# Kernel tuning notes

Measured on AMD Instinct MI355X. Metric: run time of the kernel, lower is better.

## Reference

```python
import jax, jax.numpy as jnp
import numpy as np

EPS = 1e-5


def conv2d(x, w, b, groups=1):
    # x: NCHW, w: OIHW, stride 1, SAME padding (== padding=k//2 for odd k)
    y = jax.lax.conv_general_dilated(
        x, w, window_strides=(1, 1), padding='SAME',
        dimension_numbers=('NCHW', 'OIHW', 'NCHW'),
        feature_group_count=groups)
    return y + b[None, :, None, None]


def gelu(x):
    return jax.nn.gelu(x, approximate=False)  # torch default GELU is exact erf


def adaptive_feature_norm(x, gamma, beta, s1w, s1b, s2w, s2b):
    # stats_net: GAP -> 1x1 conv -> ReLU -> 1x1 conv -> chunk into (gamma_a, beta_a)
    pooled = x.mean(axis=(2, 3), keepdims=True)                 # [B,C,1,1]
    h = jax.nn.relu(conv2d(pooled, s1w, s1b))
    stats = conv2d(h, s2w, s2b)                                 # [B,2C,1,1]
    ag, ab = jnp.split(stats, 2, axis=1)
    mean = x.mean(axis=(2, 3), keepdims=True)
    n = x.shape[2] * x.shape[3]
    var = ((x - mean) ** 2).sum(axis=(2, 3), keepdims=True) / (n - 1)  # unbiased, torch.var_mean default
    x_norm = (x - mean) * jax.lax.rsqrt(var + EPS)
    return (1 + ag) * gamma * x_norm + ab * beta


def setup_inputs() -> dict:
    key = jax.random.key(0)
    ks = jax.random.split(key, 40)
    B, C, H, W = 16, 256, 96, 96
    c4 = C // 4

    def n(k, shape, s=0.02):
        return jax.random.normal(k, shape, dtype=jnp.float32) * s

    inp = dict(
        x=jax.random.normal(ks[0], (B, C, H, W), dtype=jnp.float32),
        # branch1 conv1: dim -> dim//4, 3x3
        b1_conv1_w=n(ks[1], (c4, C, 3, 3)), b1_conv1_b=jnp.zeros((c4,), jnp.float32),
        # AFN on dim//4
        afn1_gamma=jnp.ones((1, c4, 1, 1), jnp.float32), afn1_beta=jnp.zeros((1, c4, 1, 1), jnp.float32),
        afn1_s1_w=n(ks[2], (c4 // 4, c4, 1, 1)), afn1_s1_b=jnp.zeros((c4 // 4,), jnp.float32),
        afn1_s2_w=n(ks[3], (c4 * 2, c4 // 4, 1, 1)), afn1_s2_b=jnp.zeros((c4 * 2,), jnp.float32),
        # branch1 conv2: dim//4 -> dim, 3x3
        b1_conv2_w=n(ks[4], (C, c4, 3, 3)), b1_conv2_b=jnp.zeros((C,), jnp.float32),
        # AFN on dim
        afn2_gamma=jnp.ones((1, C, 1, 1), jnp.float32), afn2_beta=jnp.zeros((1, C, 1, 1), jnp.float32),
        afn2_s1_w=n(ks[5], (c4, C, 1, 1)), afn2_s1_b=jnp.zeros((c4,), jnp.float32),
        afn2_s2_w=n(ks[6], (C * 2, c4, 1, 1)), afn2_s2_b=jnp.zeros((C * 2,), jnp.float32),
        # attention qkv/proj (1x1 convs)
        qkv_w=n(ks[7], (3 * C, C, 1, 1)), qkv_b=jnp.zeros((3 * C,), jnp.float32),
        proj_w=n(ks[8], (C, C, 1, 1)), proj_b=jnp.zeros((C,), jnp.float32),
        # 3 frequency decomposition branches, stacked
        # grouped 3x3 conv: groups=C//4, in=C (4 per group), out=C//4 (1 per group) -> weight [C//4, 4, 3, 3]
        fd_dw_w=n(ks[9], (3, c4, 4, 3, 3)), fd_dw_b=jnp.zeros((3, c4), jnp.float32),
        fd_pw_w=n(ks[10], (3, C, c4, 1, 1)), fd_pw_b=jnp.zeros((3, C), jnp.float32),
        freq_weights=jnp.ones((3,), jnp.float32),
        # router: GAP -> 1x1 conv -> softmax over 2 routes
        router_w=n(ks[11], (2, C, 1, 1)), router_b=jnp.zeros((2,), jnp.float32),
    )
    return inp


def reference(x,
              b1_conv1_w, b1_conv1_b, afn1_gamma, afn1_beta, afn1_s1_w, afn1_s1_b, afn1_s2_w, afn1_s2_b,
              b1_conv2_w, b1_conv2_b, afn2_gamma, afn2_beta, afn2_s1_w, afn2_s1_b, afn2_s2_w, afn2_s2_b,
              qkv_w, qkv_b, proj_w, proj_b, fd_dw_w, fd_dw_b, fd_pw_w, fd_pw_b, freq_weights,
              router_w, router_b):
    B, C, H, W = x.shape
    num_heads = 8
    hd = C // num_heads
    scale = C ** (-0.5)

    # ---- router ----
    pooled = x.mean(axis=(2, 3), keepdims=True)
    route = jax.nn.softmax(conv2d(pooled, router_w, router_b), axis=1)  # [B,2,1,1]

    # ---- branch1: conv -> AFN -> GELU -> conv -> AFN ----
    h = conv2d(x, b1_conv1_w, b1_conv1_b)
    h = adaptive_feature_norm(h, afn1_gamma, afn1_beta, afn1_s1_w, afn1_s1_b, afn1_s2_w, afn1_s2_b)
    h = gelu(h)
    h = conv2d(h, b1_conv2_w, b1_conv2_b)
    out1 = adaptive_feature_norm(h, afn2_gamma, afn2_beta, afn2_s1_w, afn2_s1_b, afn2_s2_w, afn2_s2_b)

    # ---- branch2: multi-scale frequency attention ----
    qkv = conv2d(x, qkv_w, qkv_b).reshape(B, 3, num_heads, hd, H, W)
    q, k, v = qkv[:, 0], qkv[:, 1], qkv[:, 2]          # [B, nh, hd, H, W]
    # attn over spatial rows: q @ k^T contracts W -> [B, nh, hd, H, H]
    attn = jnp.einsum('bndhw,bndgw->bndhg', q, k) * scale
    attn = jax.nn.softmax(attn, axis=-1)
    a = jnp.einsum('bndhg,bndgw->bndhw', attn, v)       # [B, nh, hd, H, W]
    # torch: .transpose(1, 2).reshape(B, C, H, W)  (hd-major channel order)
    a = a.transpose(0, 2, 1, 3, 4).reshape(B, C, H, W)
    x_attn = conv2d(a, proj_w, proj_b)

    fw = jax.nn.softmax(freq_weights, axis=0)
    freq_out = 0.0
    for i in range(3):
        f = conv2d(x, fd_dw_w[i], fd_dw_b[i], groups=C // 4)
        f = conv2d(gelu(f), fd_pw_w[i], fd_pw_b[i])
        freq_out = freq_out + fw[i] * f
    out2 = x_attn + freq_out

    return x + route[:, 0:1, :, :] * out1 + route[:, 1:2, :, :] * out2
```

## Files before the change

### kernel.cpp

```cpp
#include <hip/hip_runtime.h>
#include <hip/hip_bf16.h>
#include <math.h>
#include <stdint.h>

#define BB 16
#define CC 256
#define C4 64
#define HH 96
#define WW 96
#define HW 9216
#define EPSF 1e-5f

using bf16x8 = __attribute__((ext_vector_type(8))) short;
using bf16x4 = __attribute__((ext_vector_type(4))) short;
using f32x4  = __attribute__((ext_vector_type(4))) float;

#define GLD16(g, l) \
    __builtin_amdgcn_global_load_lds((const __attribute__((address_space(1))) unsigned int*)(g), \
                                     (__attribute__((address_space(3))) unsigned int*)(l), 16, 0, 0)

__device__ inline float bf2f_bits(short s) {
    return __uint_as_float(((unsigned int)(unsigned short)s) << 16);
}
__device__ inline short f2bf_bits(float f) {
    unsigned int u = __float_as_uint(f);
    return (short)((u + 0x7fffu + ((u >> 16) & 1u)) >> 16);
}

__global__ void zero_n_kernel(unsigned int* __restrict__ p, int n) {
    int i = blockIdx.x * 256 + threadIdx.x;
    if (i < n) p[i] = 0u;
}

__global__ void router_kernel(const float* __restrict__ pooled, const float* __restrict__ rw,
                              const float* __restrict__ rb, const float* __restrict__ fwts,
                              float* __restrict__ route, float* __restrict__ fw) {
    int t = threadIdx.x;
    const float invhw = 1.f / (float)HW;
    if (t < BB) {
        float l0 = rb[0], l1 = rb[1];
        for (int c = 0; c < CC; ++c) {
            float p = pooled[t * CC + c] * invhw;
            l0 += p * rw[c];
            l1 += p * rw[CC + c];
        }
        float m = fmaxf(l0, l1);
        float e0 = __expf(l0 - m), e1 = __expf(l1 - m);
        float inv = 1.f / (e0 + e1);
        route[t * 2 + 0] = e0 * inv;
        route[t * 2 + 1] = e1 * inv;
    }
    if (t == BB) {
        float a = fwts[0], b = fwts[1], c = fwts[2];
        float m = fmaxf(a, fmaxf(b, c));
        float e0 = __expf(a - m), e1 = __expf(b - m), e2 = __expf(c - m);
        float inv = 1.f / (e0 + e1 + e2);
        fw[0] = e0 * inv; fw[1] = e1 * inv; fw[2] = e2 * inv;
    }
}

__global__ void pack_w3x3_kernel(const float* __restrict__ w, __hip_bfloat16* __restrict__ wt,
                                 int COUT, int CINW) {
    int idx = blockIdx.x * 256 + threadIdx.x;
    int total = COUT * 9 * CINW;
    if (idx >= total) return;
    int ci = idx % CINW; int rest = idx / CINW; int tau = rest % 9; int co = rest / 9;
    wt[idx] = __float2bfloat16(w[((size_t)co * CINW + ci) * 9 + tau]);
}

__global__ void cast_w_kernel(const float* __restrict__ w, __hip_bfloat16* __restrict__ o, int n) {
    int idx = blockIdx.x * 256 + threadIdx.x;
    if (idx < n) o[idx] = __float2bfloat16(w[idx]);
}

__global__ void cast_w448_kernel(const float* __restrict__ w, __hip_bfloat16* __restrict__ A448) {
    int idx = blockIdx.x * 256 + threadIdx.x;
    int co = idx >> 8, ci = idx & 255;
    A448[co * 448 + ci] = __float2bfloat16(w[idx]);
}

__global__ void fuse_freq_w448_kernel(const float* __restrict__ pww, const float* __restrict__ pwb,
                                      const float* __restrict__ pjb, const float* __restrict__ fw,
                                      __hip_bfloat16* __restrict__ A448, float* __restrict__ fb448) {
    int co = blockIdx.x; int t = threadIdx.x;
    int i = t >> 6, g = t & 63;
    A448[co * 448 + 256 + t] = __float2bfloat16(fw[i] * pww[((size_t)(i * 256 + co)) * 64 + g]);
    if (t == 0) fb448[co] = pjb[co] + fw[0] * pwb[co] + fw[1] * pwb[256 + co] + fw[2] * pwb[512 + co];
}

__device__ inline float to_f32(float v) { return v; }
__device__ inline float to_f32(__hip_bfloat16 v) { return __bfloat162float(v); }

template <typename TIN, int CIN, int OSTR, bool POOL>
__global__ __launch_bounds__(256) void transpose_pm_kernel(const TIN* __restrict__ x,
                                                           __hip_bfloat16* __restrict__ xt,
                                                           float* __restrict__ pooled) {
    __shared__ float s[32][33];
    __shared__ float ps[8][32];
    int p0 = blockIdx.x * 32, c0 = blockIdx.y * 32, b = blockIdx.z;
    int tx = threadIdx.x, ty = threadIdx.y;
    const TIN* xp = x + ((size_t)b * CIN + c0) * HW + p0;
#pragma unroll
    for (int i = 0; i < 4; ++i) {
        int c = ty * 4 + i;
        s[c][tx] = to_f32(xp[(size_t)c * HW + tx]);
    }
    __syncthreads();
    __hip_bfloat16* yp = xt + ((size_t)b * HW + p0) * OSTR + c0;
#pragma unroll
    for (int i = 0; i < 4; ++i) {
        int r = ty * 4 + i;
        yp[(size_t)r * OSTR + tx] = __float2bfloat16(s[tx][r]);
    }
    if (POOL) {
        float l4 = 0.f;
#pragma unroll
        for (int i = 0; i < 4; ++i) l4 += s[tx][ty * 4 + i];
        ps[ty][tx] = l4;
        __syncthreads();
        if (ty == 0) {
            float tot = 0.f;
#pragma unroll
            for (int k = 0; k < 8; ++k) tot += ps[k][tx];
            atomicAdd(&pooled[b * CIN + c0 + tx], tot);
        }
    }
}

template <int BM, int BN, int TSH, int KC, int CDIM, int EPI, int CO_TOT, bool STATS>
__global__ __launch_bounds__(256) void mfma_gemm_kernel(const short* __restrict__ A,
                                                        const short* __restrict__ Bx,
                                                        const short* __restrict__ zp,
                                                        const float* __restrict__ bias,
                                                        const float* __restrict__ route,
                                                        void* __restrict__ Y,
                                                        float* __restrict__ ssum,
                                                        float* __restrict__ sssq,
                                                        int bin0, int bout0) {
    constexpr int WM = BM / 2, WN = BN / 2;
    constexpr int FM = WM / 16, FN = WN / 16;
    constexpr int KB = KC / 32;
    constexpr int NA = BM / 16;
    constexpr int NB = BN / 16;
    __shared__ __align__(16) short As[BM * 32];
    __shared__ __align__(16) short Bs[BN * 32];
    int tid = threadIdx.x;
    int wid = tid >> 6, lane = tid & 63;
    int wy = wid >> 1, wx = wid & 1;
    int lane16 = lane & 15, quad = lane >> 4;
    int lrow = lane >> 2, lchk = lane & 3;
    int co0 = blockIdx.x * BM;
    int n0 = blockIdx.y * BN;
    int bin = blockIdx.z + bin0;
    int bout = blockIdx.z + bout0;

    f32x4 acc[FM][FN];
#pragma unroll
    for (int i = 0; i < FM; ++i)
#pragma unroll
        for (int j = 0; j < FN; ++j) acc[i][j] = (f32x4){0.f, 0.f, 0.f, 0.f};

    const short* Bbase = Bx + (size_t)bin * HW * CDIM;

    for (int tau = 0; tau < TSH; ++tau) {
        int dh = tau / 3, dw = tau % 3;
        int off = (TSH > 1) ? (dh - 1) * 96 + (dw - 1) : 0;
        for (int kb = 0; kb < KB; ++kb) {
            int kc0 = kb * 32;
#pragma unroll
            for (int t = 0; t < NA / 4; ++t) {
                int inst = wid * (NA / 4) + t;
                int row = inst * 16 + lrow;
                const short* g = A + (size_t)(co0 + row) * (TSH * KC) + tau * KC + kc0 + lchk * 8;
                GLD16(g, &As[inst * 512]);
            }
#pragma unroll
            for (int t = 0; t < NB / 4; ++t) {
                int inst = wid * (NB / 4) + t;
                int row = inst * 16 + lrow;
                int n = n0 + row;
                const short* g;
                if (TSH > 1) {
                    int h = n / 96, w = n - h * 96;
                    int hh = h + dh - 1, ww2 = w + dw - 1;
                    bool valid = ((unsigned)hh < 96u) && ((unsigned)ww2 < 96u);
                    g = valid ? (Bbase + (size_t)(n + off) * CDIM + kc0 + lchk * 8) : zp;
                } else {
                    g = Bbase + (size_t)n * CDIM + kc0 + lchk * 8;
                }
                GLD16(g, &Bs[inst * 512]);
            }
            __syncthreads();
            bf16x8 af[FM], bfr[FN];
#pragma unroll
            for (int i = 0; i < FM; ++i)
                af[i] = *(const bf16x8*)&As[(wy * WM + i * 16 + lane16) * 32 + quad * 8];
#pragma unroll
            for (int j = 0; j < FN; ++j)
                bfr[j] = *(const bf16x8*)&Bs[(wx * WN + j * 16 + lane16) * 32 + quad * 8];
#pragma unroll
            for (int i = 0; i < FM; ++i)
#pragma unroll
                for (int j = 0; j < FN; ++j)
                    acc[i][j] = __builtin_amdgcn_mfma_f32_16x16x32_bf16(af[i], bfr[j], acc[i][j], 0, 0, 0);
            __syncthreads();
        }
    }
    float scale = 1.f;
    if (EPI == 2) scale = route[bin * 2 + 1];
    float sl[FM][4], ql[FM][4];
    if (STATS) {
#pragma unroll
        for (int i = 0; i < FM; ++i)
#pragma unroll
            for (int r = 0; r < 4; ++r) { sl[i][r] = 0.f; ql[i][r] = 0.f; }
    }
#pragma unroll
    for (int i = 0; i < FM; ++i) {
        int co_l = co0 + wy * WM + i * 16 + quad * 4;
#pragma unroll
        for (int j = 0; j < FN; ++j) {
            int pix = n0 + wx * WN + j * 16 + lane16;
#pragma unroll
            for (int r = 0; r < 4; ++r) {
                int co = co_l + r;
                float v = acc[i][j][r] + bias[co];
                size_t idx = ((size_t)(bout * CO_TOT + co)) * HW + pix;
                if (EPI == 0) ((float*)Y)[idx] = v;
                else if (EPI == 1) ((__hip_bfloat16*)Y)[idx] = __float2bfloat16(v);
                else ((float*)Y)[idx] += scale * v;
                if (STATS) { sl[i][r] += v; ql[i][r] += v * v; }
            }
        }
    }
    if (STATS) {
#pragma unroll
        for (int i = 0; i < FM; ++i) {
            int co_l = co0 + wy * WM + i * 16 + quad * 4;
#pragma unroll
            for (int r = 0; r < 4; ++r) {
                float s = sl[i][r], q = ql[i][r];
                s += __shfl_xor(s, 1); q += __shfl_xor(q, 1);
                s += __shfl_xor(s, 2); q += __shfl_xor(q, 2);
                s += __shfl_xor(s, 4); q += __shfl_xor(q, 4);
                s += __shfl_xor(s, 8); q += __shfl_xor(q, 8);
                if (lane16 == 0) {
                    int bc = bout * CO_TOT + co_l + r;
                    atomicAdd(&ssum[bc], s);
                    atomicAdd(&sssq[bc], q);
                }
            }
        }
    }
}

__global__ void afn_finalize_kernel(const float* __restrict__ s, const float* __restrict__ q,
                                    float* __restrict__ mean, float* __restrict__ istd, int n) {
    int i = blockIdx.x * 256 + threadIdx.x;
    if (i >= n) return;
    float m = s[i] / (float)HW;
    float var = (q[i] - s[i] * m) / (float)(HW - 1);
    mean[i] = m;
    istd[i] = rsqrtf(var + EPSF);
}

template <int CH, int HID>
__global__ void afn_mlp_kernel(const float* __restrict__ mean,
                               const float* __restrict__ s1w, const float* __restrict__ s1b,
                               const float* __restrict__ s2w, const float* __restrict__ s2b,
                               float* __restrict__ ag, float* __restrict__ ab) {
    int b = blockIdx.x;
    __shared__ float hbuf[HID];
    int t = threadIdx.x;
    if (t < HID) {
        float s = s1b[t];
        for (int c = 0; c < CH; ++c) s += mean[b * CH + c] * s1w[t * CH + c];
        hbuf[t] = fmaxf(s, 0.f);
    }
    __syncthreads();
    if (t < 2 * CH) {
        float s = s2b[t];
#pragma unroll
        for (int k = 0; k < HID; ++k) s += hbuf[k] * s2w[t * HID + k];
        if (t < CH) ag[b * CH + t] = s;
        else        ab[b * CH + (t - CH)] = s;
    }
}

template <int CH, bool GELU>
__global__ void afn_apply_kernel(float* __restrict__ hbuf_g, const float* __restrict__ mean,
                                 const float* __restrict__ istd, const float* __restrict__ ag,
                                 const float* __restrict__ ab, const float* __restrict__ gamma,
                                 const float* __restrict__ beta) {
    int p = blockIdx.x * 256 + threadIdx.x;
    int c = blockIdx.y, b = blockIdx.z;
    int bc = b * CH + c;
    float scale = (1.f + ag[bc]) * gamma[c] * istd[bc];
    float shift = ab[bc] * beta[c];
    float m = mean[bc];
    float* ptr = hbuf_g + (size_t)bc * HW + p;
    float v = (*ptr - m) * scale + shift;
    if (GELU) v = 0.5f * v * (1.f + erff(v * 0.70710678118654752f));
    *ptr = v;
}

__global__ __launch_bounds__(256) void afn_combine_kernel(const float* __restrict__ x,
                                                          const float* __restrict__ h2,
                                                          const float* __restrict__ mean,
                                                          const float* __restrict__ istd,
                                                          const float* __restrict__ ag,
                                                          const float* __restrict__ ab,
                                                          const float* __restrict__ gamma,
                                                          const float* __restrict__ beta,
                                                          const float* __restrict__ route,
                                                          float* __restrict__ out) {
    int p4 = blockIdx.x * 256 + threadIdx.x;
    int c = blockIdx.y, b = blockIdx.z;
    int bc = b * CC + c;
    float scale = (1.f + ag[bc]) * gamma[c] * istd[bc];
    float shift = ab[bc] * beta[c];
    float m = mean[bc];
    float r0 = route[b * 2];
    size_t base = (size_t)bc * (HW / 4) + p4;
    const f32x4 xv = ((const f32x4*)x)[base];
    const f32x4 hv = ((const f32x4*)h2)[base];
    f32x4 o;
#pragma unroll
    for (int e = 0; e < 4; ++e) o[e] = xv[e] + r0 * ((hv[e] - m) * scale + shift);
    ((f32x4*)out)[base] = o;
}

__global__ __launch_bounds__(256) void vtrans_kernel(const __hip_bfloat16* __restrict__ qkv,
                                                     __hip_bfloat16* __restrict__ vt) {
    __shared__ __hip_bfloat16 s[32][34];
    int th = blockIdx.x / 3, tw = blockIdx.x % 3;
    int c = blockIdx.y, b = blockIdx.z;
    int tx = threadIdx.x, ty = threadIdx.y;
    const __hip_bfloat16* ip = qkv + ((size_t)b * 768 + 512 + c) * HW + (size_t)(th * 32) * 96 + tw * 32;
#pragma unroll
    for (int i = 0; i < 4; ++i) s[ty * 4 + i][tx] = ip[(size_t)(ty * 4 + i) * 96 + tx];
    __syncthreads();
    __hip_bfloat16* op = vt + ((size_t)b * 256 + c) * HW + (size_t)(tw * 32) * 96 + th * 32;
#pragma unroll
    for (int i = 0; i < 4; ++i) op[(size_t)(ty * 4 + i) * 96 + tx] = s[tx][ty * 4 + i];
}

__global__ __launch_bounds__(256) void attn_mfma_kernel(const __hip_bfloat16* __restrict__ qkv,
                                                        const __hip_bfloat16* __restrict__ vt,
                                                        __hip_bfloat16* __restrict__ a, int bout0) {
    int d = blockIdx.x, n = blockIdx.y, b = blockIdx.z;
    __shared__ __align__(16) __hip_bfloat16 Ps[96 * 104];
    int t = threadIdx.x;
    int lane = t & 63, wid = t >> 6;
    int wy = wid >> 1, wx = wid & 1;
    int lane16 = lane & 15, quad = lane >> 4;

    const __hip_bfloat16* qp = qkv + ((size_t)b * 768 + n * 32 + d) * HW;
    const __hip_bfloat16* kp = qp + (size_t)256 * HW;
    const __hip_bfloat16* vp = vt + ((size_t)b * 256 + n * 32 + d) * HW;

    f32x4 acc[3][3];
#pragma unroll
    for (int i = 0; i < 3; ++i)
#pragma unroll
        for (int j = 0; j < 3; ++j) acc[i][j] = (f32x4){0.f, 0.f, 0.f, 0.f};

#pragma unroll
    for (int kb = 0; kb < 3; ++kb) {
        int kc = kb * 32 + quad * 8;
        bf16x8 af[3], bfr[3];
#pragma unroll
        for (int i = 0; i < 3; ++i)
            af[i] = *(const bf16x8*)(qp + (size_t)(wy * 48 + i * 16 + lane16) * 96 + kc);
#pragma unroll
        for (int j = 0; j < 3; ++j)
            bfr[j] = *(const bf16x8*)(kp + (size_t)(wx * 48 + j * 16 + lane16) * 96 + kc);
#pragma unroll
        for (int i = 0; i < 3; ++i)
#pragma unroll
            for (int j = 0; j < 3; ++j)
                acc[i][j] = __builtin_amdgcn_mfma_f32_16x16x32_bf16(af[i], bfr[j], acc[i][j], 0, 0, 0);
    }

    const float scale = 0.0625f;
#pragma unroll
    for (int i = 0; i < 3; ++i) {
        int rbase = wy * 48 + i * 16 + quad * 4;
#pragma unroll
        for (int j = 0; j < 3; ++j) {
            int col = wx * 48 + j * 16 + lane16;
#pragma unroll
            for (int r = 0; r < 4; ++r)
                Ps[(rbase + r) * 104 + col] = __float2bfloat16(acc[i][j][r] * scale);
        }
    }
    __syncthreads();

    if (t < 192) {
        int row = t >> 1, hh = t & 1;
        const bf16x4* pr4 = (const bf16x4*)&Ps[row * 104 + hh * 48];
        float vb[48];
        float m = -1e30f;
#pragma unroll
        for (int j4 = 0; j4 < 12; ++j4) {
            bf16x4 u = pr4[j4];
#pragma unroll
            for (int e = 0; e < 4; ++e) {
                float f = bf2f_bits(u[e]);
                vb[j4 * 4 + e] = f;
                m = fmaxf(m, f);
            }
        }
        m = fmaxf(m, __shfl_xor(m, 1));
        float ssum = 0.f;
#pragma unroll
        for (int j2 = 0; j2 < 48; ++j2) { vb[j2] = __expf(vb[j2] - m); ssum += vb[j2]; }
        ssum += __shfl_xor(ssum, 1);
        float inv = 1.f / ssum;
        bf16x4* pw4 = (bf16x4*)&Ps[row * 104 + hh * 48];
#pragma unroll
        for (int j4 = 0; j4 < 12; ++j4) {
            bf16x4 o;
#pragma unroll
            for (int e = 0; e < 4; ++e) o[e] = f2bf_bits(vb[j4 * 4 + e] * inv);
            pw4[j4] = o;
        }
    }
    __syncthreads();

#pragma unroll
    for (int i = 0; i < 3; ++i)
#pragma unroll
        for (int j = 0; j < 3; ++j) acc[i][j] = (f32x4){0.f, 0.f, 0.f, 0.f};

#pragma unroll
    for (int kb = 0; kb < 3; ++kb) {
        int kc = kb * 32 + quad * 8;
        bf16x8 af[3], bfr[3];
#pragma unroll
        for (int i = 0; i < 3; ++i)
            af[i] = *(const bf16x8*)&Ps[(wy * 48 + i * 16 + lane16) * 104 + kc];
#pragma unroll
        for (int j = 0; j < 3; ++j)
            bfr[j] = *(const bf16x8*)(vp + (size_t)(wx * 48 + j * 16 + lane16) * 96 + kc);
#pragma unroll
        for (int i = 0; i < 3; ++i)
#pragma unroll
            for (int j = 0; j < 3; ++j)
                acc[i][j] = __builtin_amdgcn_mfma_f32_16x16x32_bf16(af[i], bfr[j], acc[i][j], 0, 0, 0);
    }

    __hip_bfloat16* ap = a + ((size_t)(bout0 + b) * CC + (d * 8 + n)) * HW;
#pragma unroll
    for (int i = 0; i < 3; ++i) {
        int rbase = wy * 48 + i * 16 + quad * 4;
#pragma unroll
        for (int j = 0; j < 3; ++j) {
            int col = wx * 48 + j * 16 + lane16;
#pragma unroll
            for (int r = 0; r < 4; ++r)
                ap[(size_t)(rbase + r) * 96 + col] = __float2bfloat16(acc[i][j][r]);
        }
    }
}

__global__ __launch_bounds__(256) void freq3_kernel(const float* __restrict__ x,
                                                    const float* __restrict__ dww,
                                                    const float* __restrict__ dwb,
                                                    __hip_bfloat16* __restrict__ f) {
    int p = blockIdx.x * 256 + threadIdx.x;
    int g = blockIdx.y;
    int b = blockIdx.z;
    int h = p / WW, w = p % WW;
    float a0 = dwb[g], a1 = dwb[64 + g], a2 = dwb[128 + g];
    const float* w0 = dww + g * 36;
    const float* w1 = dww + (64 + g) * 36;
    const float* w2 = dww + (128 + g) * 36;
#pragma unroll
    for (int q = 0; q < 4; ++q) {
        const float* xc = x + ((size_t)b * CC + 4 * g + q) * HW;
#pragma unroll
        for (int dh = 0; dh < 3; ++dh) {
            int hh = h + dh - 1;
            bool hv = (hh >= 0) && (hh < HH);
#pragma unroll
            for (int dw = 0; dw < 3; ++dw) {
                int ww2 = w + dw - 1;
                bool v = hv && (ww2 >= 0) && (ww2 < WW);
                float xv = v ? xc[hh * WW + ww2] : 0.f;
                int wi = q * 9 + dh * 3 + dw;
                a0 += xv * w0[wi];
                a1 += xv * w1[wi];
                a2 += xv * w2[wi];
            }
        }
    }
    a0 = 0.5f * a0 * (1.f + erff(a0 * 0.70710678118654752f));
    a1 = 0.5f * a1 * (1.f + erff(a1 * 0.70710678118654752f));
    a2 = 0.5f * a2 * (1.f + erff(a2 * 0.70710678118654752f));
    size_t base = ((size_t)b * 192 + g) * HW + p;
    f[base] = __float2bfloat16(a0);
    f[base + (size_t)64 * HW] = __float2bfloat16(a1);
    f[base + (size_t)128 * HW] = __float2bfloat16(a2);
}

extern "C" void kernel_launch(void* const* d_in, const int* in_sizes, int n_in,
                              void* d_out, int out_size, void* d_ws, size_t ws_size,
                              hipStream_t stream) {
    const float* x    = (const float*)d_in[0];
    const float* c1w  = (const float*)d_in[1];
    const float* c1b  = (const float*)d_in[2];
    const float* g1   = (const float*)d_in[3];
    const float* be1  = (const float*)d_in[4];
    const float* s1w1 = (const float*)d_in[5];
    const float* s1b1 = (const float*)d_in[6];
    const float* s2w1 = (const float*)d_in[7];
    const float* s2b1 = (const float*)d_in[8];
    const float* c2w  = (const float*)d_in[9];
    const float* c2b  = (const float*)d_in[10];
    const float* g2   = (const float*)d_in[11];
    const float* be2  = (const float*)d_in[12];
    const float* s1w2 = (const float*)d_in[13];
    const float* s1b2 = (const float*)d_in[14];
    const float* s2w2 = (const float*)d_in[15];
    const float* s2b2 = (const float*)d_in[16];
    const float* qkvw = (const float*)d_in[17];
    const float* qkvb = (const float*)d_in[18];
    const float* pjw  = (const float*)d_in[19];
    const float* pjb  = (const float*)d_in[20];
    const float* dww  = (const float*)d_in[21];
    const float* dwb  = (const float*)d_in[22];
    const float* pww  = (const float*)d_in[23];
    const float* pwb  = (const float*)d_in[24];
    const float* fwts = (const float*)d_in[25];
    const float* rw   = (const float*)d_in[26];
    const float* rb   = (const float*)d_in[27];
    float* out = (float*)d_out;
    (void)ws_size;

    char* ws = (char*)d_ws;
    float* h2 = (float*)ws;
    __hip_bfloat16* qkvs = (__hip_bfloat16*)ws;
    __hip_bfloat16* fall = (__hip_bfloat16*)ws;
    __hip_bfloat16* ftA = (__hip_bfloat16*)(ws + 56623104ULL);
    __hip_bfloat16* vt = (__hip_bfloat16*)(ws + 113246208ULL);
    float* h1 = (float*)(ws + 150994944ULL);
    __hip_bfloat16* h1t = (__hip_bfloat16*)(ws + 188743680ULL);
    __hip_bfloat16* xt = (__hip_bfloat16*)(ws + 207618048ULL);
    __hip_bfloat16* at = xt;
    const size_t TB = 283115520ULL;
    short* zp = (short*)(ws + TB);
    float* zf = (float*)(ws + TB + 256);
    float* ssum1  = zf;
    float* sssq1  = zf + 1024;
    float* ssum2  = zf + 2048;
    float* sssq2  = zf + 6144;
    float* pooled = zf + 10240;
    float* route  = zf + 14336;
    float* fw     = zf + 14368;
    float* mean1  = zf + 14372;
    float* istd1  = zf + 15396;
    float* ag1    = zf + 16420;
    float* ab1    = zf + 17444;
    float* mean2  = zf + 18468;
    float* istd2  = zf + 22564;
    float* ag2    = zf + 26660;
    float* ab2    = zf + 30756;
    float* fb448  = zf + 34852;
    char* wbase = (char*)(zf + 35108);
    __hip_bfloat16* wt1  = (__hip_bfloat16*)wbase;
    __hip_bfloat16* wt2  = (__hip_bfloat16*)(wbase + 294912);
    __hip_bfloat16* qw16 = (__hip_bfloat16*)(wbase + 589824);
    __hip_bfloat16* A448 = (__hip_bfloat16*)(wbase + 983040);

    zero_n_kernel<<<57, 256, 0, stream>>>((unsigned int*)zp, 14400);

    transpose_pm_kernel<float, 256, 256, true>
        <<<dim3(288, 8, 16), dim3(32, 8), 0, stream>>>(x, xt, pooled);
    router_kernel<<<1, 64, 0, stream>>>(pooled, rw, rb, fwts, route, fw);

    pack_w3x3_kernel<<<576, 256, 0, stream>>>(c1w, wt1, 64, 256);
    pack_w3x3_kernel<<<576, 256, 0, stream>>>(c2w, wt2, 256, 64);
    cast_w_kernel<<<768, 256, 0, stream>>>(qkvw, qw16, 768 * 256);
    cast_w448_kernel<<<256, 256, 0, stream>>>(pjw, A448);
    fuse_freq_w448_kernel<<<256, 192, 0, stream>>>(pww, pwb, pjb, fw, A448, fb448);

    mfma_gemm_kernel<64, 128, 9, 256, 256, 0, 64, true>
        <<<dim3(1, 72, 16), 256, 0, stream>>>((const short*)wt1, (const short*)xt, zp, c1b,
                                              nullptr, h1, ssum1, sssq1, 0, 0);
    afn_finalize_kernel<<<4, 256, 0, stream>>>(ssum1, sssq1, mean1, istd1, BB * C4);
    afn_mlp_kernel<64, 16><<<dim3(BB), 128, 0, stream>>>(mean1, s1w1, s1b1, s2w1, s2b1, ag1, ab1);
    afn_apply_kernel<64, true><<<dim3(36, 64, 16), 256, 0, stream>>>(h1, mean1, istd1, ag1, ab1, g1, be1);
    transpose_pm_kernel<float, 64, 64, false>
        <<<dim3(288, 2, 16), dim3(32, 8), 0, stream>>>(h1, h1t, nullptr);
    mfma_gemm_kernel<128, 128, 9, 64, 64, 0, 256, true>
        <<<dim3(2, 72, 16), 256, 0, stream>>>((const short*)wt2, (const short*)h1t, zp, c2b,
                                              nullptr, h2, ssum2, sssq2, 0, 0);
    afn_finalize_kernel<<<16, 256, 0, stream>>>(ssum2, sssq2, mean2, istd2, BB * CC);
    afn_mlp_kernel<256, 64><<<dim3(BB), 512, 0, stream>>>(mean2, s1w2, s1b2, s2w2, s2b2, ag2, ab2);
    afn_combine_kernel<<<dim3(9, 256, 16), 256, 0, stream>>>(x, h2, mean2, istd2, ag2, ab2,
                                                             g2, be2, route, out);

    for (int half = 0; half < 2; ++half) {
        mfma_gemm_kernel<128, 128, 1, 256, 256, 1, 768, false>
            <<<dim3(6, 72, 8), 256, 0, stream>>>((const short*)qw16, (const short*)xt, zp, qkvb,
                                                 nullptr, qkvs, nullptr, nullptr, half * 8, 0);
        vtrans_kernel<<<dim3(9, 256, 8), dim3(32, 8), 0, stream>>>(qkvs, vt);
        attn_mfma_kernel<<<dim3(32, 8, 8), 256, 0, stream>>>(qkvs, vt, at, half * 8);
    }

    freq3_kernel<<<dim3(36, 64, 16), 256, 0, stream>>>(x, dww, dwb, fall);

    transpose_pm_kernel<__hip_bfloat16, 256, 448, false>
        <<<dim3(288, 8, 16), dim3(32, 8), 0, stream>>>(at, ftA, nullptr);
    transpose_pm_kernel<__hip_bfloat16, 192, 448, false>
        <<<dim3(288, 6, 16), dim3(32, 8), 0, stream>>>(fall, ftA + 256, nullptr);

    mfma_gemm_kernel<128, 128, 1, 448, 448, 2, 256, false>
        <<<dim3(2, 72, 16), 256, 0, stream>>>((const short*)A448, (const short*)ftA, zp, fb448,
                                              route, out, nullptr, nullptr, 0, 0);
}
```

Before: 1.224 ms.

## Double-buffer GEMM LDS with swizzle and fuse AFN+GELU into transpose

The MFMA GEMM main loop now double-buffers LDS tiles and processes 64-wide K steps. The next stage's global-to-LDS loads are issued while the current stage computes, which halves the number of barriers. A XOR swizzle on the 16-byte chunk index is applied to both the LDS writes and reads to reduce bank conflicts. Separately, the standalone AFN-apply+GELU pass over h1 is folded into the transpose kernel, removing one full read/write of the 64-channel activation. In exchange, LDS use quadruples, which may lower occupancy, and all K dimensions must be multiples of 64.

```diff
diff --git a/kernel.cpp b/kernel.cpp
--- a/kernel.cpp
+++ b/kernel.cpp
@@ -91,10 +91,16 @@
 __device__ inline float to_f32(float v) { return v; }
 __device__ inline float to_f32(__hip_bfloat16 v) { return __bfloat162float(v); }
 
-template <typename TIN, int CIN, int OSTR, bool POOL>
+template <typename TIN, int CIN, int OSTR, bool POOL, bool AFN, bool GELU>
 __global__ __launch_bounds__(256) void transpose_pm_kernel(const TIN* __restrict__ x,
                                                            __hip_bfloat16* __restrict__ xt,
-                                                           float* __restrict__ pooled) {
+                                                           float* __restrict__ pooled,
+                                                           const float* __restrict__ mean,
+                                                           const float* __restrict__ istd,
+                                                           const float* __restrict__ ag,
+                                                           const float* __restrict__ ab,
+                                                           const float* __restrict__ gamma,
+                                                           const float* __restrict__ beta) {
     __shared__ float s[32][33];
     __shared__ float ps[8][32];
     int p0 = blockIdx.x * 32, c0 = blockIdx.y * 32, b = blockIdx.z;
@@ -103,7 +109,15 @@
 #pragma unroll
     for (int i = 0; i < 4; ++i) {
         int c = ty * 4 + i;
-        s[c][tx] = to_f32(xp[(size_t)c * HW + tx]);
+        float v = to_f32(xp[(size_t)c * HW + tx]);
+        if (AFN) {
+            int bc = b * CIN + c0 + c;
+            float sc = (1.f + ag[bc]) * gamma[c0 + c] * istd[bc];
+            float sh = ab[bc] * beta[c0 + c];
+            v = (v - mean[bc]) * sc + sh;
+            if (GELU) v = 0.5f * v * (1.f + erff(v * 0.70710678118654752f));
+        }
+        s[c][tx] = v;
     }
     __syncthreads();
     __hip_bfloat16* yp = xt + ((size_t)b * HW + p0) * OSTR + c0;
@@ -139,16 +153,18 @@
                                                         int bin0, int bout0) {
     constexpr int WM = BM / 2, WN = BN / 2;
     constexpr int FM = WM / 16, FN = WN / 16;
-    constexpr int KB = KC / 32;
+    constexpr int KBT = KC / 64;
+    constexpr int NS = TSH * KBT;
     constexpr int NA = BM / 16;
     constexpr int NB = BN / 16;
-    __shared__ __align__(16) short As[BM * 32];
-    __shared__ __align__(16) short Bs[BN * 32];
+    __shared__ __align__(16) short As[2][2][BM * 32];
+    __shared__ __align__(16) short Bs[2][2][BN * 32];
     int tid = threadIdx.x;
     int wid = tid >> 6, lane = tid & 63;
     int wy = wid >> 1, wx = wid & 1;
     int lane16 = lane & 15, quad = lane >> 4;
     int lrow = lane >> 2, lchk = lane & 3;
+    int swz = (lrow >> 1) & 3;
     int co0 = blockIdx.x * BM;
     int n0 = blockIdx.y * BN;
     int bin = blockIdx.z + bin0;
@@ -162,17 +178,21 @@
 
     const short* Bbase = Bx + (size_t)bin * HW * CDIM;
 
-    for (int tau = 0; tau < TSH; ++tau) {
+    auto stage = [&](int s, int d) {
+        int tau = (TSH > 1) ? (s / KBT) : 0;
+        int kb  = s - tau * KBT;
+        int kc0 = kb * 64;
         int dh = tau / 3, dw = tau % 3;
-        int off = (TSH > 1) ? (dh - 1) * 96 + (dw - 1) : 0;
-        for (int kb = 0; kb < KB; ++kb) {
-            int kc0 = kb * 32;
+        int off = (dh - 1) * 96 + (dw - 1);
+        int ksw = kc0 + (lchk ^ swz) * 8;
+#pragma unroll
+        for (int kk = 0; kk < 2; ++kk) {
 #pragma unroll
             for (int t = 0; t < NA / 4; ++t) {
                 int inst = wid * (NA / 4) + t;
                 int row = inst * 16 + lrow;
-                const short* g = A + (size_t)(co0 + row) * (TSH * KC) + tau * KC + kc0 + lchk * 8;
-                GLD16(g, &As[inst * 512]);
+                const short* g = A + (size_t)(co0 + row) * (TSH * KC) + tau * KC + ksw + kk * 32;
+                GLD16(g, &As[d][kk][inst * 512]);
             }
 #pragma unroll
             for (int t = 0; t < NB / 4; ++t) {
@@ -184,28 +204,44 @@
                     int h = n / 96, w = n - h * 96;
                     int hh = h + dh - 1, ww2 = w + dw - 1;
                     bool valid = ((unsigned)hh < 96u) && ((unsigned)ww2 < 96u);
-                    g = valid ? (Bbase + (size_t)(n + off) * CDIM + kc0 + lchk * 8) : zp;
+                    g = valid ? (Bbase + (size_t)(n + off) * CDIM + ksw + kk * 32) : zp;
                 } else {
-                    g = Bbase + (size_t)n * CDIM + kc0 + lchk * 8;
+                    g = Bbase + (size_t)n * CDIM + ksw + kk * 32;
                 }
-                GLD16(g, &Bs[inst * 512]);
-            }
-            __syncthreads();
+                GLD16(g, &Bs[d][kk][inst * 512]);
+            }
+        }
+    };
+
+    stage(0, 0);
+    __syncthreads();
+    for (int s = 0; s < NS; ++s) {
+        int cur = s & 1;
+        if (s + 1 < NS) stage(s + 1, cur ^ 1);
+#pragma unroll
+        for (int kk = 0; kk < 2; ++kk) {
             bf16x8 af[FM], bfr[FN];
 #pragma unroll
-            for (int i = 0; i < FM; ++i)
-                af[i] = *(const bf16x8*)&As[(wy * WM + i * 16 + lane16) * 32 + quad * 8];
-#pragma unroll
-            for (int j = 0; j < FN; ++j)
-                bfr[j] = *(const bf16x8*)&Bs[(wx * WN + j * 16 + lane16) * 32 + quad * 8];
+            for (int i = 0; i < FM; ++i) {
+                int row = wy * WM + i * 16 + lane16;
+                int ch = (quad ^ ((row >> 1) & 3)) * 8;
+                af[i] = *(const bf16x8*)&As[cur][kk][row * 32 + ch];
+            }
+#pragma unroll
+            for (int j = 0; j < FN; ++j) {
+                int row = wx * WN + j * 16 + lane16;
+                int ch = (quad ^ ((row >> 1) & 3)) * 8;
+                bfr[j] = *(const bf16x8*)&Bs[cur][kk][row * 32 + ch];
+            }
 #pragma unroll
             for (int i = 0; i < FM; ++i)
 #pragma unroll
                 for (int j = 0; j < FN; ++j)
                     acc[i][j] = __builtin_amdgcn_mfma_f32_16x16x32_bf16(af[i], bfr[j], acc[i][j], 0, 0, 0);
-            __syncthreads();
-        }
-    }
+        }
+        __syncthreads();
+    }
+
     float scale = 1.f;
     if (EPI == 2) scale = route[bin * 2 + 1];
     float sl[FM][4], ql[FM][4];
@@ -285,23 +321,6 @@
         if (t < CH) ag[b * CH + t] = s;
         else        ab[b * CH + (t - CH)] = s;
     }
-}
-
-template <int CH, bool GELU>
-__global__ void afn_apply_kernel(float* __restrict__ hbuf_g, const float* __restrict__ mean,
-                                 const float* __restrict__ istd, const float* __restrict__ ag,
-                                 const float* __restrict__ ab, const float* __restrict__ gamma,
-                                 const float* __restrict__ beta) {
-    int p = blockIdx.x * 256 + threadIdx.x;
-    int c = blockIdx.y, b = blockIdx.z;
-    int bc = b * CH + c;
-    float scale = (1.f + ag[bc]) * gamma[c] * istd[bc];
-    float shift = ab[bc] * beta[c];
-    float m = mean[bc];
-    float* ptr = hbuf_g + (size_t)bc * HW + p;
-    float v = (*ptr - m) * scale + shift;
-    if (GELU) v = 0.5f * v * (1.f + erff(v * 0.70710678118654752f));
-    *ptr = v;
 }
 
 __global__ __launch_bounds__(256) void afn_combine_kernel(const float* __restrict__ x,
@@ -575,8 +594,9 @@
 
     zero_n_kernel<<<57, 256, 0, stream>>>((unsigned int*)zp, 14400);
 
-    transpose_pm_kernel<float, 256, 256, true>
-        <<<dim3(288, 8, 16), dim3(32, 8), 0, stream>>>(x, xt, pooled);
+    transpose_pm_kernel<float, 256, 256, true, false, false>
+        <<<dim3(288, 8, 16), dim3(32, 8), 0, stream>>>(x, xt, pooled, nullptr, nullptr,
+                                                       nullptr, nullptr, nullptr, nullptr);
     router_kernel<<<1, 64, 0, stream>>>(pooled, rw, rb, fwts, route, fw);
 
     pack_w3x3_kernel<<<576, 256, 0, stream>>>(c1w, wt1, 64, 256);
@@ -590,9 +610,9 @@
                                               nullptr, h1, ssum1, sssq1, 0, 0);
     afn_finalize_kernel<<<4, 256, 0, stream>>>(ssum1, sssq1, mean1, istd1, BB * C4);
     afn_mlp_kernel<64, 16><<<dim3(BB), 128, 0, stream>>>(mean1, s1w1, s1b1, s2w1, s2b1, ag1, ab1);
-    afn_apply_kernel<64, true><<<dim3(36, 64, 16), 256, 0, stream>>>(h1, mean1, istd1, ag1, ab1, g1, be1);
-    transpose_pm_kernel<float, 64, 64, false>
-        <<<dim3(288, 2, 16), dim3(32, 8), 0, stream>>>(h1, h1t, nullptr);
+    transpose_pm_kernel<float, 64, 64, false, true, true>
+        <<<dim3(288, 2, 16), dim3(32, 8), 0, stream>>>(h1, h1t, nullptr, mean1, istd1,
+                                                       ag1, ab1, g1, be1);
     mfma_gemm_kernel<128, 128, 9, 64, 64, 0, 256, true>
         <<<dim3(2, 72, 16), 256, 0, stream>>>((const short*)wt2, (const short*)h1t, zp, c2b,
                                               nullptr, h2, ssum2, sssq2, 0, 0);
@@ -611,10 +631,12 @@
 
     freq3_kernel<<<dim3(36, 64, 16), 256, 0, stream>>>(x, dww, dwb, fall);
 
-    transpose_pm_kernel<__hip_bfloat16, 256, 448, false>
-        <<<dim3(288, 8, 16), dim3(32, 8), 0, stream>>>(at, ftA, nullptr);
-    transpose_pm_kernel<__hip_bfloat16, 192, 448, false>
-        <<<dim3(288, 6, 16), dim3(32, 8), 0, stream>>>(fall, ftA + 256, nullptr);
+    transpose_pm_kernel<__hip_bfloat16, 256, 448, false, false, false>
+        <<<dim3(288, 8, 16), dim3(32, 8), 0, stream>>>(at, ftA, nullptr, nullptr, nullptr,
+                                                       nullptr, nullptr, nullptr, nullptr);
+    transpose_pm_kernel<__hip_bfloat16, 192, 448, false, false, false>
+        <<<dim3(288, 6, 16), dim3(32, 8), 0, stream>>>(fall, ftA + 256, nullptr, nullptr, nullptr,
+                                                       nullptr, nullptr, nullptr, nullptr);
 
     mfma_gemm_kernel<128, 128, 1, 448, 448, 2, 256, false>
         <<<dim3(2, 72, 16), 256, 0, stream>>>((const short*)A448, (const short*)ftA, zp, fb448,
```

After: 1.224 ms. No clear change (-0.0%).
